# Optimization experiments

Hardware: AMD Instinct MI355X
Metric: run time of the kernel (lower is better)

## Reference

```python
import jax, jax.numpy as jnp
import numpy as np

N_NODES = 100000
N_EDGES = 1000000
N_INPUT = 64
N_HIDDEN = 64
K = 8


def setup_inputs() -> dict:
    key = jax.random.key(0)
    k1, k2, k3, k4 = jax.random.split(key, 4)
    x = jax.random.normal(k1, (N_NODES, N_INPUT), dtype=jnp.float32)
    edge_index = jax.random.randint(k2, (2, N_EDGES), 0, N_NODES, dtype=jnp.int64)
    # ChebConv has K independent [in, out] weight matrices (Glorot-ish scale) and a bias.
    weight = jax.random.normal(k3, (K, N_INPUT, N_HIDDEN), dtype=jnp.float32) * (1.0 / np.sqrt(N_INPUT))
    bias = jax.random.normal(k4, (N_HIDDEN,), dtype=jnp.float32) * 0.01
    return {"x": x, "edge_index": edge_index, "weight": weight, "bias": bias}


def _cheb_edge_norm(edge_index, num_nodes):
    # PyG ChebConv sym normalization with default lambda_max=2.0:
    #   L_hat = (2/lambda_max) * (I - D^-1/2 A D^-1/2) - I = -D^-1/2 A D^-1/2
    # (the diagonal +1 from the Laplacian and the -1 self-loop cancel exactly).
    src, dst = edge_index[0], edge_index[1]
    ones = jnp.ones(src.shape[0], dtype=jnp.float32)
    deg = jax.ops.segment_sum(ones, src, num_segments=num_nodes)
    deg_inv_sqrt = jnp.where(deg > 0, jax.lax.rsqrt(jnp.maximum(deg, 1.0)), 0.0)
    return -deg_inv_sqrt[src] * deg_inv_sqrt[dst]  # [E]


def reference(x, edge_index, weight, bias):
    num_nodes = x.shape[0]
    src, dst = edge_index[0], edge_index[1]
    norm = _cheb_edge_norm(edge_index, num_nodes)

    def prop(h):  # h: [N, F] -> L_hat @ h via gather-multiply-scatter over edges
        return jax.ops.segment_sum(norm[:, None] * h[src], dst, num_segments=num_nodes)

    # Chebyshev recursion: T0 = x, T1 = L_hat x, Tk = 2 L_hat T_{k-1} - T_{k-2}
    Tx0 = x
    out = Tx0 @ weight[0]
    Tx1 = prop(Tx0)
    out = out + Tx1 @ weight[1]
    for k in range(2, weight.shape[0]):
        Tx2 = 2.0 * prop(Tx1) - Tx0
        out = out + Tx2 @ weight[k]
        Tx0, Tx1 = Tx1, Tx2
    out = out + bias
    # bn=False path: ReLU then dropout (identity in eval mode)
    return jax.nn.relu(out)
```

## Files before the change

### kernel.cpp

```cpp
#include <hip/hip_runtime.h>
#include <hip/hip_bf16.h>

typedef __attribute__((ext_vector_type(8))) short s16x8;
typedef __attribute__((ext_vector_type(4))) float f32x4;

#define HC 48
#define RBH 6400
#define RBS 3200

static __device__ __forceinline__ unsigned short f2bf(float f) {
    unsigned int u = __float_as_uint(f);
    unsigned int r = (u + 0x7FFFu + ((u >> 16) & 1u)) >> 16;
    return (unsigned short)r;
}

__global__ __launch_bounds__(256) void k_hist(const int* __restrict__ eidx,
                                              unsigned short* __restrict__ partials,
                                              int N, int E, int HR) {
    __shared__ int h[RBH];
    int b = blockIdx.x;
    int job = b / (HR * HC);
    int rc = b % (HR * HC);
    int r = rc / HC, c = rc % HC;
    int lo = r * RBH;
    int nb = min(RBH, N - lo);
    if (nb <= 0) return;
    for (int i = threadIdx.x; i < nb; i += 256) h[i] = 0;
    __syncthreads();
    const int* vals = eidx + (size_t)job * E;
    int e0 = (int)(((long long)E * c / HC) & ~3LL);
    int e1 = (c == HC - 1) ? E : (int)(((long long)E * (c + 1) / HC) & ~3LL);
    int e = e0 + threadIdx.x * 4;
    for (; e + 4 <= e1; e += 1024) {
        int4 v = *reinterpret_cast<const int4*>(vals + e);
        unsigned r0 = (unsigned)(v.x - lo), r1 = (unsigned)(v.y - lo);
        unsigned r2 = (unsigned)(v.z - lo), r3 = (unsigned)(v.w - lo);
        if (r0 < (unsigned)nb) atomicAdd(&h[r0], 1);
        if (r1 < (unsigned)nb) atomicAdd(&h[r1], 1);
        if (r2 < (unsigned)nb) atomicAdd(&h[r2], 1);
        if (r3 < (unsigned)nb) atomicAdd(&h[r3], 1);
    }
    if (threadIdx.x == 0)
        for (int t = e1 & ~3; t < e1; ++t) {
            unsigned rel = (unsigned)(vals[t] - lo);
            if (rel < (unsigned)nb) atomicAdd(&h[rel], 1);
        }
    __syncthreads();
    unsigned short* outp = partials + ((size_t)(job * HC + c)) * N + lo;
    for (int i = threadIdx.x; i < nb; i += 256) outp[i] = (unsigned short)h[i];
}

__global__ __launch_bounds__(1024) void k_rs(const unsigned short* __restrict__ partials,
                                             float* __restrict__ dis,
                                             int* __restrict__ cnt,
                                             int* __restrict__ incl,
                                             int* __restrict__ bsum, int N) {
    __shared__ int sm[1024];
    int t = threadIdx.x;
    int i = blockIdx.x * 1024 + t;
    int csum = 0;
    if (i < N) {
        int dsum = 0;
        for (int c = 0; c < HC; ++c) {
            dsum += partials[(size_t)c * N + i];
            csum += partials[(size_t)(HC + c) * N + i];
        }
        dis[i] = dsum > 0 ? rsqrtf((float)dsum) : 0.f;
        cnt[i] = csum;
    }
    sm[t] = (i < N) ? csum : 0;
    __syncthreads();
    for (int off = 1; off < 1024; off <<= 1) {
        int add = (t >= off) ? sm[t - off] : 0;
        __syncthreads();
        sm[t] += add;
        __syncthreads();
    }
    if (i < N) incl[i] = sm[t];
    if (t == 1023) bsum[blockIdx.x] = sm[1023];
}

__global__ __launch_bounds__(1024) void k_scan3(const int* __restrict__ cnt,
                                                const int* __restrict__ bsum,
                                                int* __restrict__ rowptr,
                                                const unsigned short* __restrict__ pdst,
                                                int* __restrict__ cbase, int N, int nb) {
    __shared__ int sb[128];
    int t = threadIdx.x;
    if (t < 128) sb[t] = (t < nb) ? bsum[t] : 0;
    __syncthreads();
    for (int off = 1; off < 128; off <<= 1) {
        int add = (t < 128 && t >= off) ? sb[t - off] : 0;
        __syncthreads();
        if (t < 128) sb[t] += add;
        __syncthreads();
    }
    int b = blockIdx.x;
    int boff = (b == 0) ? 0 : sb[b - 1];
    int total = sb[nb - 1];
    int i = b * 1024 + t;
    if (i >= N) return;
    int ex = rowptr[i] - cnt[i] + boff;
    rowptr[i] = ex;
    if (i == N - 1) rowptr[N] = total;
    int run = ex;
    for (int c = 0; c < HC; ++c) {
        size_t idx = (size_t)c * N + i;
        cbase[idx] = run;
        run += pdst[idx];
    }
}

__global__ __launch_bounds__(256) void k_scatter(
        const int* __restrict__ src, const int* __restrict__ dst,
        const int* __restrict__ cbase, int* __restrict__ srcs, int N, int E) {
    __shared__ int cur[RBS];
    int r = blockIdx.x / HC, c = blockIdx.x % HC;
    int lo = r * RBS;
    int nb = min(RBS, N - lo);
    if (nb <= 0) return;
    for (int i = threadIdx.x; i < nb; i += 256)
        cur[i] = cbase[(size_t)c * N + lo + i];
    __syncthreads();
    int e0 = (int)(((long long)E * c / HC) & ~3LL);
    int e1 = (c == HC - 1) ? E : (int)(((long long)E * (c + 1) / HC) & ~3LL);
    int e = e0 + threadIdx.x * 4;
    for (; e + 4 <= e1; e += 1024) {
        int4 d4 = *reinterpret_cast<const int4*>(dst + e);
        unsigned r0 = (unsigned)(d4.x - lo), r1 = (unsigned)(d4.y - lo);
        unsigned r2 = (unsigned)(d4.z - lo), r3 = (unsigned)(d4.w - lo);
        if (r0 < (unsigned)nb) srcs[atomicAdd(&cur[r0], 1)] = src[e];
        if (r1 < (unsigned)nb) srcs[atomicAdd(&cur[r1], 1)] = src[e + 1];
        if (r2 < (unsigned)nb) srcs[atomicAdd(&cur[r2], 1)] = src[e + 2];
        if (r3 < (unsigned)nb) srcs[atomicAdd(&cur[r3], 1)] = src[e + 3];
    }
    if (threadIdx.x == 0)
        for (int t = e1 & ~3; t < e1; ++t) {
            unsigned rel = (unsigned)(dst[t] - lo);
            if (rel < (unsigned)nb) srcs[atomicAdd(&cur[rel], 1)] = src[t];
        }
}

__global__ void k_pack(const float* __restrict__ x, const float* __restrict__ dis,
                       const float* __restrict__ W,
                       unsigned short* __restrict__ tb0, unsigned short* __restrict__ ysA,
                       unsigned short* __restrict__ ysB, unsigned short* __restrict__ wt,
                       int N, int K) {
    int t = blockIdx.x * blockDim.x + threadIdx.x;
    int nys = (N + 1) * 32;
    if (t < nys) {
        int row = t >> 5, p = t & 31;
        size_t o = ((size_t)row << 6) + (p << 1);
        if (row == N) {
            *(unsigned*)(ysA + o) = 0;
            *(unsigned*)(ysB + o) = 0;
            return;
        }
        float2 v = *reinterpret_cast<const float2*>(x + o);
        float dv = dis[row];
        *(unsigned*)(tb0 + o) = (unsigned)f2bf(v.x) | ((unsigned)f2bf(v.y) << 16);
        *(unsigned*)(ysA + o) = (unsigned)f2bf(v.x * dv) | ((unsigned)f2bf(v.y * dv) << 16);
    } else {
        int u = t - nys;
        if (u < K * 4096) {
            float v = W[u];
            int k = u >> 12;
            int r = u & 4095;
            int i = r >> 6;
            int j = r & 63;
            wt[(size_t)j * (K * 64) + (k << 6) + i] = f2bf(v);
        }
    }
}

static __device__ __forceinline__ void addrow(float* acc, uint4 t) {
    acc[0] += __uint_as_float(t.x << 16);
    acc[1] += __uint_as_float(t.x & 0xffff0000u);
    acc[2] += __uint_as_float(t.y << 16);
    acc[3] += __uint_as_float(t.y & 0xffff0000u);
    acc[4] += __uint_as_float(t.z << 16);
    acc[5] += __uint_as_float(t.z & 0xffff0000u);
    acc[6] += __uint_as_float(t.w << 16);
    acc[7] += __uint_as_float(t.w & 0xffff0000u);
}

__global__ __launch_bounds__(256) void k_prop(
        const unsigned short* __restrict__ Ysin,
        const unsigned short* __restrict__ Tm2,
        unsigned short* __restrict__ Tout,
        unsigned short* __restrict__ Ysout,
        const int* __restrict__ rowptr, const int* __restrict__ srcs,
        const float* __restrict__ dis,
        int N, int E, float scale, float beta, int wys) {
    int gt = blockIdx.x * blockDim.x + threadIdx.x;
    int wave0 = (gt >> 6) << 3;
    int lane = gt & 63;
    int g = lane >> 3;
    int i = lane & 7;
    int node = wave0 + g;
    bool live = node < N;
    int rs = 0, deg = 0;
    if (live) {
        rs = rowptr[node];
        deg = rowptr[node + 1] - rs;
    }
    int wmax = deg;
#pragma unroll
    for (int m = 8; m <= 32; m <<= 1) {
        int o = __shfl_xor(wmax, m);
        wmax = o > wmax ? o : wmax;
    }
    float acc[8];
#pragma unroll
    for (int j = 0; j < 8; ++j) acc[j] = 0.f;
    for (int e = 0; e < wmax; e += 8) {
        int b = rs + e;
        int s[8];
#pragma unroll
        for (int q = 0; q < 8; ++q)
            s[q] = (e + q < deg) ? srcs[min(b + q, E - 1)] : N;
        uint4 t[8];
#pragma unroll
        for (int q = 0; q < 8; ++q)
            t[q] = *reinterpret_cast<const uint4*>(Ysin + ((size_t)s[q] << 6) + (i << 3));
#pragma unroll
        for (int q = 0; q < 8; ++q) addrow(acc, t[q]);
    }
    if (live) {
        float dv = dis[node];
        float sc = -scale * dv;
        size_t base = ((size_t)node << 6) + (i << 3);
        float r[8];
#pragma unroll
        for (int j = 0; j < 8; ++j) r[j] = sc * acc[j];
        if (beta != 0.f) {
            uint4 pv = *reinterpret_cast<const uint4*>(Tm2 + base);
            r[0] = fmaf(beta, __uint_as_float(pv.x << 16), r[0]);
            r[1] = fmaf(beta, __uint_as_float(pv.x & 0xffff0000u), r[1]);
            r[2] = fmaf(beta, __uint_as_float(pv.y << 16), r[2]);
            r[3] = fmaf(beta, __uint_as_float(pv.y & 0xffff0000u), r[3]);
            r[4] = fmaf(beta, __uint_as_float(pv.z << 16), r[4]);
            r[5] = fmaf(beta, __uint_as_float(pv.z & 0xffff0000u), r[5]);
            r[6] = fmaf(beta, __uint_as_float(pv.w << 16), r[6]);
            r[7] = fmaf(beta, __uint_as_float(pv.w & 0xffff0000u), r[7]);
        }
        uint4 ov;
        ov.x = (unsigned)f2bf(r[0]) | ((unsigned)f2bf(r[1]) << 16);
        ov.y = (unsigned)f2bf(r[2]) | ((unsigned)f2bf(r[3]) << 16);
        ov.z = (unsigned)f2bf(r[4]) | ((unsigned)f2bf(r[5]) << 16);
        ov.w = (unsigned)f2bf(r[6]) | ((unsigned)f2bf(r[7]) << 16);
        *reinterpret_cast<uint4*>(Tout + base) = ov;
        if (wys) {
            uint4 yv;
            yv.x = (unsigned)f2bf(r[0] * dv) | ((unsigned)f2bf(r[1] * dv) << 16);
            yv.y = (unsigned)f2bf(r[2] * dv) | ((unsigned)f2bf(r[3] * dv) << 16);
            yv.z = (unsigned)f2bf(r[4] * dv) | ((unsigned)f2bf(r[5] * dv) << 16);
            yv.w = (unsigned)f2bf(r[6] * dv) | ((unsigned)f2bf(r[7] * dv) << 16);
            *reinterpret_cast<uint4*>(Ysout + base) = yv;
        }
    }
}

template <int KS>
__global__ __launch_bounds__(256) void k_gemm(const unsigned short* __restrict__ tb,
                                              const unsigned short* __restrict__ wt,
                                              const float* __restrict__ bias,
                                              float* __restrict__ out,
                                              int N, int NF) {
    constexpr int NB = KS / 2;
    __shared__ unsigned short lds[KS * 512];
    int lane = threadIdx.x & 63;
    int w = threadIdx.x >> 6;
    int l16 = lane & 15;
    int quad = lane >> 4;
    const int KI = KS * 32;

    s16x8 afr[KS];
    {
        const unsigned short* wrow = wt + (size_t)(w * 16 + l16) * KI + quad * 8;
#pragma unroll
        for (int ks = 0; ks < KS; ++ks)
            afr[ks] = *reinterpret_cast<const s16x8*>(wrow + ks * 32);
    }
    f32x4 bias4 = *reinterpret_cast<const f32x4*>(bias + w * 16 + quad * 4);

    int ntiles = N >> 4;
    for (int t = blockIdx.x; t < ntiles; t += gridDim.x) {
        const char* tilebase = (const char*)tb + (size_t)t * 2048;
#pragma unroll
        for (int inst = 0; inst < 2 * NB; ++inst) {
            if ((inst & 3) != w) continue;
            int kbuf = inst >> 1;
            int j = inst & 1;
            int p = j * 64 + lane;
            int nrow = p >> 3;
            int s = (p & 7) ^ (nrow & 7);
            const char* g = tilebase + (size_t)kbuf * NF * 2 + nrow * 128 + s * 16;
            __builtin_amdgcn_global_load_lds(
                (const __attribute__((address_space(1))) unsigned int*)g,
                (__attribute__((address_space(3))) unsigned int*)(lds + inst * 512),
                16, 0, 0);
        }
        __syncthreads();
        f32x4 acc = {0.f, 0.f, 0.f, 0.f};
#pragma unroll
        for (int ks = 0; ks < KS; ++ks) {
            int kbuf = ks >> 1, half = ks & 1;
            int sph = (half * 4 + quad) ^ (l16 & 7);
            s16x8 bf = *reinterpret_cast<const s16x8*>(
                lds + kbuf * 1024 + l16 * 64 + sph * 8);
            acc = __builtin_amdgcn_mfma_f32_16x16x32_bf16(afr[ks], bf, acc, 0, 0, 0);
        }
        float* orow = out + (size_t)(t * 16 + l16) * 64 + w * 16 + quad * 4;
        f32x4 r;
#pragma unroll
        for (int q = 0; q < 4; ++q) {
            float v = acc[q] + bias4[q];
            r[q] = v > 0.f ? v : 0.f;
        }
        *reinterpret_cast<f32x4*>(orow) = r;
        __syncthreads();
    }
}

extern "C" void kernel_launch(void* const* d_in, const int* in_sizes, int n_in,
                              void* d_out, int out_size, void* d_ws, size_t ws_size,
                              hipStream_t stream) {
    const float* x    = (const float*)d_in[0];
    const int*   eidx = (const int*)d_in[1];
    const float* W    = (const float*)d_in[2];
    const float* bias = (const float*)d_in[3];
    float* out = (float*)d_out;

    const int NF = in_sizes[0];
    const int N  = NF / 64;
    const int E  = in_sizes[1] / 2;
    const int K  = in_sizes[2] / 4096;

    const int* src = eidx;
    const int* dst = eidx + E;

    char* ws = (char*)d_ws;
    size_t off = 0;
    auto alloc = [&](size_t bytes) -> char* {
        char* p = ws + off;
        off = (off + bytes + 255) & ~(size_t)255;
        return p;
    };
    unsigned short* Tb = (unsigned short*)alloc((size_t)K * NF * 2);
    unsigned short* Ys[2];
    Ys[0] = (unsigned short*)alloc((size_t)(N + 1) * 64 * 2);
    Ys[1] = (unsigned short*)alloc((size_t)(N + 1) * 64 * 2);
    unsigned short* Wt = (unsigned short*)alloc((size_t)64 * K * 64 * 2);
    int*   srcs   = (int*)alloc((size_t)E * 4);
    int*   rowptr = (int*)alloc((size_t)(N + 1) * 4);
    int*   cnt    = (int*)alloc((size_t)N * 4);
    unsigned short* partials = (unsigned short*)alloc((size_t)2 * HC * N * 2);
    int*   cbase  = (int*)alloc((size_t)HC * N * 4);
    float* dis  = (float*)alloc((size_t)N * 4);
    int*   bsum = (int*)alloc(1024);
    (void)ws_size; (void)n_in; (void)out_size;

    int HR = (N + RBH - 1) / RBH;
    int SR = (N + RBS - 1) / RBS;
    const unsigned short* pdst = partials + (size_t)HC * N;

    k_hist<<<2 * HR * HC, 256, 0, stream>>>(eidx, partials, N, E, HR);
    int nb = (N + 1023) / 1024;
    k_rs<<<nb, 1024, 0, stream>>>(partials, dis, cnt, rowptr, bsum, N);
    k_scan3<<<nb, 1024, 0, stream>>>(cnt, bsum, rowptr, pdst, cbase, N, nb);
    k_scatter<<<SR * HC, 256, 0, stream>>>(src, dst, cbase, srcs, N, E);
    int packn = (N + 1) * 32 + K * 4096;
    k_pack<<<(packn + 255) / 256, 256, 0, stream>>>(x, dis, W, Tb, Ys[0], Ys[1], Wt, N, K);

    int waves = (N + 7) / 8;
    int pblocks = (waves * 64 + 255) / 256;
    for (int p = 1; p < K; ++p) {
        float scale = (p == 1) ? 1.f : 2.f;
        float beta  = (p == 1) ? 0.f : -1.f;
        const unsigned short* Tm2 = Tb + (size_t)(p >= 2 ? p - 2 : 0) * NF;
        k_prop<<<pblocks, 256, 0, stream>>>(
            Ys[(p - 1) & 1], Tm2, Tb + (size_t)p * NF, Ys[p & 1],
            rowptr, srcs, dis, N, E, scale, beta, p < K - 1 ? 1 : 0);
    }

    if (K == 8)      k_gemm<16><<<1024, 256, 0, stream>>>(Tb, Wt, bias, out, N, NF);
    else if (K == 4) k_gemm<8><<<1024, 256, 0, stream>>>(Tb, Wt, bias, out, N, NF);
    else if (K == 2) k_gemm<4><<<1024, 256, 0, stream>>>(Tb, Wt, bias, out, N, NF);
    else if (K == 1) k_gemm<2><<<1024, 256, 0, stream>>>(Tb, Wt, bias, out, N, NF);
}
```

Measured before the change: 334.5 us.

## Propagate degree-scaled features only and rescale by sqrt(deg) in the GEMM epilogue

The Chebyshev recursion now runs on Y_k = D^-1/2 T_k, so each propagation step writes one bf16 tensor instead of both T_k and Y_k. The final GEMM multiplies by sqrt(deg) per row in its epilogue. Nodes with zero degree take a separate path using x and a precombined alternating-sign weight sum. This cuts store traffic in every k_prop pass and drops the separate T buffers, at the cost of an extra sqrt array, a per-row branch in the GEMM, and a possible change in bf16 rounding behaviour.

```diff
diff --git a/kernel.cpp b/kernel.cpp
--- a/kernel.cpp
+++ b/kernel.cpp
@@ -52,6 +52,7 @@
 
 __global__ __launch_bounds__(1024) void k_rs(const unsigned short* __restrict__ partials,
                                              float* __restrict__ dis,
+                                             float* __restrict__ dsi,
                                              int* __restrict__ cnt,
                                              int* __restrict__ incl,
                                              int* __restrict__ bsum, int N) {
@@ -66,6 +67,7 @@
             csum += partials[(size_t)(HC + c) * N + i];
         }
         dis[i] = dsum > 0 ? rsqrtf((float)dsum) : 0.f;
+        dsi[i] = dsum > 0 ? sqrtf((float)dsum) : 0.f;
         cnt[i] = csum;
     }
     sm[t] = (i < N) ? csum : 0;
@@ -143,23 +145,22 @@
 
 __global__ void k_pack(const float* __restrict__ x, const float* __restrict__ dis,
                        const float* __restrict__ W,
-                       unsigned short* __restrict__ tb0, unsigned short* __restrict__ ysA,
-                       unsigned short* __restrict__ ysB, unsigned short* __restrict__ wt,
-                       int N, int K) {
+                       unsigned short* __restrict__ ysb, unsigned short* __restrict__ wt,
+                       float* __restrict__ walt,
+                       int N, int K, int PSE) {
     int t = blockIdx.x * blockDim.x + threadIdx.x;
     int nys = (N + 1) * 32;
     if (t < nys) {
         int row = t >> 5, p = t & 31;
+        if (row == N) {
+            for (int k = 0; k < K; ++k)
+                *(unsigned*)(ysb + (size_t)k * PSE + ((size_t)N << 6) + (p << 1)) = 0;
+            return;
+        }
         size_t o = ((size_t)row << 6) + (p << 1);
-        if (row == N) {
-            *(unsigned*)(ysA + o) = 0;
-            *(unsigned*)(ysB + o) = 0;
-            return;
-        }
         float2 v = *reinterpret_cast<const float2*>(x + o);
         float dv = dis[row];
-        *(unsigned*)(tb0 + o) = (unsigned)f2bf(v.x) | ((unsigned)f2bf(v.y) << 16);
-        *(unsigned*)(ysA + o) = (unsigned)f2bf(v.x * dv) | ((unsigned)f2bf(v.y * dv) << 16);
+        *(unsigned*)(ysb + o) = (unsigned)f2bf(v.x * dv) | ((unsigned)f2bf(v.y * dv) << 16);
     } else {
         int u = t - nys;
         if (u < K * 4096) {
@@ -169,6 +170,12 @@
             int i = r >> 6;
             int j = r & 63;
             wt[(size_t)j * (K * 64) + (k << 6) + i] = f2bf(v);
+        } else if (u < K * 4096 + 4096) {
+            int u2 = u - K * 4096;
+            float s = 0.f;
+            for (int k = 0; k < K; k += 2)
+                s += ((k & 3) == 0 ? 1.f : -1.f) * W[k * 4096 + u2];
+            walt[u2] = s;
         }
     }
 }
@@ -186,12 +193,11 @@
 
 __global__ __launch_bounds__(256) void k_prop(
         const unsigned short* __restrict__ Ysin,
-        const unsigned short* __restrict__ Tm2,
-        unsigned short* __restrict__ Tout,
+        const unsigned short* __restrict__ Ysm2,
         unsigned short* __restrict__ Ysout,
         const int* __restrict__ rowptr, const int* __restrict__ srcs,
         const float* __restrict__ dis,
-        int N, int E, float scale, float beta, int wys) {
+        int N, int E, float scale, float beta) {
     int gt = blockIdx.x * blockDim.x + threadIdx.x;
     int wave0 = (gt >> 6) << 3;
     int lane = gt & 63;
@@ -228,13 +234,13 @@
     }
     if (live) {
         float dv = dis[node];
-        float sc = -scale * dv;
+        float sc = -scale * dv * dv;
         size_t base = ((size_t)node << 6) + (i << 3);
         float r[8];
 #pragma unroll
         for (int j = 0; j < 8; ++j) r[j] = sc * acc[j];
         if (beta != 0.f) {
-            uint4 pv = *reinterpret_cast<const uint4*>(Tm2 + base);
+            uint4 pv = *reinterpret_cast<const uint4*>(Ysm2 + base);
             r[0] = fmaf(beta, __uint_as_float(pv.x << 16), r[0]);
             r[1] = fmaf(beta, __uint_as_float(pv.x & 0xffff0000u), r[1]);
             r[2] = fmaf(beta, __uint_as_float(pv.y << 16), r[2]);
@@ -249,15 +255,7 @@
         ov.y = (unsigned)f2bf(r[2]) | ((unsigned)f2bf(r[3]) << 16);
         ov.z = (unsigned)f2bf(r[4]) | ((unsigned)f2bf(r[5]) << 16);
         ov.w = (unsigned)f2bf(r[6]) | ((unsigned)f2bf(r[7]) << 16);
-        *reinterpret_cast<uint4*>(Tout + base) = ov;
-        if (wys) {
-            uint4 yv;
-            yv.x = (unsigned)f2bf(r[0] * dv) | ((unsigned)f2bf(r[1] * dv) << 16);
-            yv.y = (unsigned)f2bf(r[2] * dv) | ((unsigned)f2bf(r[3] * dv) << 16);
-            yv.z = (unsigned)f2bf(r[4] * dv) | ((unsigned)f2bf(r[5] * dv) << 16);
-            yv.w = (unsigned)f2bf(r[6] * dv) | ((unsigned)f2bf(r[7] * dv) << 16);
-            *reinterpret_cast<uint4*>(Ysout + base) = yv;
-        }
+        *reinterpret_cast<uint4*>(Ysout + base) = ov;
     }
 }
 
@@ -265,8 +263,11 @@
 __global__ __launch_bounds__(256) void k_gemm(const unsigned short* __restrict__ tb,
                                               const unsigned short* __restrict__ wt,
                                               const float* __restrict__ bias,
+                                              const float* __restrict__ dsi,
+                                              const float* __restrict__ x,
+                                              const float* __restrict__ walt,
                                               float* __restrict__ out,
-                                              int N, int NF) {
+                                              int N, int PSE) {
     constexpr int NB = KS / 2;
     __shared__ unsigned short lds[KS * 512];
     int lane = threadIdx.x & 63;
@@ -295,7 +296,7 @@
             int p = j * 64 + lane;
             int nrow = p >> 3;
             int s = (p & 7) ^ (nrow & 7);
-            const char* g = tilebase + (size_t)kbuf * NF * 2 + nrow * 128 + s * 16;
+            const char* g = tilebase + (size_t)kbuf * PSE * 2 + nrow * 128 + s * 16;
             __builtin_amdgcn_global_load_lds(
                 (const __attribute__((address_space(1))) unsigned int*)g,
                 (__attribute__((address_space(3))) unsigned int*)(lds + inst * 512),
@@ -311,12 +312,27 @@
                 lds + kbuf * 1024 + l16 * 64 + sph * 8);
             acc = __builtin_amdgcn_mfma_f32_16x16x32_bf16(afr[ks], bf, acc, 0, 0, 0);
         }
-        float* orow = out + (size_t)(t * 16 + l16) * 64 + w * 16 + quad * 4;
+        int row = t * 16 + l16;
+        float dvi = dsi[row];
+        float* orow = out + (size_t)row * 64 + w * 16 + quad * 4;
         f32x4 r;
-#pragma unroll
-        for (int q = 0; q < 4; ++q) {
-            float v = acc[q] + bias4[q];
-            r[q] = v > 0.f ? v : 0.f;
+        if (dvi != 0.f) {
+#pragma unroll
+            for (int q = 0; q < 4; ++q) {
+                float v = fmaf(acc[q], dvi, bias4[q]);
+                r[q] = v > 0.f ? v : 0.f;
+            }
+        } else {
+            const float* xr = x + (size_t)row * 64;
+            float rr[4] = {bias4[0], bias4[1], bias4[2], bias4[3]};
+            for (int j = 0; j < 64; ++j) {
+                float xv = xr[j];
+                const float* wr = walt + j * 64 + w * 16 + quad * 4;
+#pragma unroll
+                for (int q = 0; q < 4; ++q) rr[q] = fmaf(xv, wr[q], rr[q]);
+            }
+#pragma unroll
+            for (int q = 0; q < 4; ++q) r[q] = rr[q] > 0.f ? rr[q] : 0.f;
         }
         *reinterpret_cast<f32x4*>(orow) = r;
         __syncthreads();
@@ -340,6 +356,8 @@
     const int* src = eidx;
     const int* dst = eidx + E;
 
+    const int PSE = (N + 1) * 64;
+
     char* ws = (char*)d_ws;
     size_t off = 0;
     auto alloc = [&](size_t bytes) -> char* {
@@ -347,17 +365,16 @@
         off = (off + bytes + 255) & ~(size_t)255;
         return p;
     };
-    unsigned short* Tb = (unsigned short*)alloc((size_t)K * NF * 2);
-    unsigned short* Ys[2];
-    Ys[0] = (unsigned short*)alloc((size_t)(N + 1) * 64 * 2);
-    Ys[1] = (unsigned short*)alloc((size_t)(N + 1) * 64 * 2);
+    unsigned short* Ysb = (unsigned short*)alloc((size_t)K * PSE * 2);
     unsigned short* Wt = (unsigned short*)alloc((size_t)64 * K * 64 * 2);
+    float* Walt  = (float*)alloc(4096 * 4);
     int*   srcs   = (int*)alloc((size_t)E * 4);
     int*   rowptr = (int*)alloc((size_t)(N + 1) * 4);
     int*   cnt    = (int*)alloc((size_t)N * 4);
     unsigned short* partials = (unsigned short*)alloc((size_t)2 * HC * N * 2);
     int*   cbase  = (int*)alloc((size_t)HC * N * 4);
     float* dis  = (float*)alloc((size_t)N * 4);
+    float* dsi  = (float*)alloc((size_t)N * 4);
     int*   bsum = (int*)alloc(1024);
     (void)ws_size; (void)n_in; (void)out_size;
 
@@ -367,25 +384,26 @@
 
     k_hist<<<2 * HR * HC, 256, 0, stream>>>(eidx, partials, N, E, HR);
     int nb = (N + 1023) / 1024;
-    k_rs<<<nb, 1024, 0, stream>>>(partials, dis, cnt, rowptr, bsum, N);
+    k_rs<<<nb, 1024, 0, stream>>>(partials, dis, dsi, cnt, rowptr, bsum, N);
     k_scan3<<<nb, 1024, 0, stream>>>(cnt, bsum, rowptr, pdst, cbase, N, nb);
     k_scatter<<<SR * HC, 256, 0, stream>>>(src, dst, cbase, srcs, N, E);
-    int packn = (N + 1) * 32 + K * 4096;
-    k_pack<<<(packn + 255) / 256, 256, 0, stream>>>(x, dis, W, Tb, Ys[0], Ys[1], Wt, N, K);
+    int packn = (N + 1) * 32 + K * 4096 + 4096;
+    k_pack<<<(packn + 255) / 256, 256, 0, stream>>>(x, dis, W, Ysb, Wt, Walt, N, K, PSE);
 
     int waves = (N + 7) / 8;
     int pblocks = (waves * 64 + 255) / 256;
     for (int p = 1; p < K; ++p) {
         float scale = (p == 1) ? 1.f : 2.f;
         float beta  = (p == 1) ? 0.f : -1.f;
-        const unsigned short* Tm2 = Tb + (size_t)(p >= 2 ? p - 2 : 0) * NF;
+        const unsigned short* Ysin = Ysb + (size_t)(p - 1) * PSE;
+        const unsigned short* Ysm2 = Ysb + (size_t)(p >= 2 ? p - 2 : 0) * PSE;
         k_prop<<<pblocks, 256, 0, stream>>>(
-            Ys[(p - 1) & 1], Tm2, Tb + (size_t)p * NF, Ys[p & 1],
-            rowptr, srcs, dis, N, E, scale, beta, p < K - 1 ? 1 : 0);
-    }
-
-    if (K == 8)      k_gemm<16><<<1024, 256, 0, stream>>>(Tb, Wt, bias, out, N, NF);
-    else if (K == 4) k_gemm<8><<<1024, 256, 0, stream>>>(Tb, Wt, bias, out, N, NF);
-    else if (K == 2) k_gemm<4><<<1024, 256, 0, stream>>>(Tb, Wt, bias, out, N, NF);
-    else if (K == 1) k_gemm<2><<<1024, 256, 0, stream>>>(Tb, Wt, bias, out, N, NF);
-}
+            Ysin, Ysm2, Ysb + (size_t)p * PSE,
+            rowptr, srcs, dis, N, E, scale, beta);
+    }
+
+    if (K == 8)      k_gemm<16><<<1024, 256, 0, stream>>>(Ysb, Wt, bias, dsi, x, Walt, out, N, PSE);
+    else if (K == 4) k_gemm<8><<<1024, 256, 0, stream>>>(Ysb, Wt, bias, dsi, x, Walt, out, N, PSE);
+    else if (K == 2) k_gemm<4><<<1024, 256, 0, stream>>>(Ysb, Wt, bias, dsi, x, Walt, out, N, PSE);
+    else if (K == 1) k_gemm<2><<<1024, 256, 0, stream>>>(Ysb, Wt, bias, dsi, x, Walt, out, N, PSE);
+}
```

After: 334.6 us. Within noise of the previous version (+0.0%).
